# Kernel optimization log

Hardware: AMD Instinct MI355X
Metric: run time of the kernel (lower is better)

## Reference

```python
import jax, jax.numpy as jnp
import numpy as np

N_AGENTS = 16
OBS = 128
STATE = 256
EMBED = 32
NHID = 32
NHEADS = 4
ALPHA = 0.2  # leaky relu slope
NEG = -9.0e15


def gat_layer(h, adj, W, a):
    # h: [B,N,Fin], W: [Fin,Fout], a: [2*Fout,1]  (dropout is identity in eval mode)
    Wh = h @ W                                   # [B,N,Fout]
    f = W.shape[1]
    e = jax.nn.leaky_relu(Wh @ a[:f] + jnp.swapaxes(Wh @ a[f:], 1, 2), ALPHA)  # [B,N,N]
    att = jnp.where(adj > 0, e, NEG)
    att = jax.nn.softmax(att, axis=1)            # faithful to torch dim=1 on [B,N,N]
    return att @ Wh                              # [B,N,Fout]


def gat(x, adj, Wh_heads, a_heads, Wout, aout):
    # Wh_heads: [H,Fin,NHID], a_heads: [H,2*NHID,1]
    heads = jax.vmap(gat_layer, in_axes=(None, None, 0, 0))(x, adj, Wh_heads, a_heads)  # [H,B,N,NHID]
    heads = jax.nn.elu(heads)                    # concat=True layers apply elu
    B, N = x.shape[0], x.shape[1]
    xcat = jnp.transpose(heads, (1, 2, 0, 3)).reshape(B, N, -1)  # [B,N,H*NHID]
    out = gat_layer(xcat, adj, Wout, aout)       # concat=False: no elu inside layer
    out = jax.nn.elu(out)
    return jax.nn.log_softmax(out, axis=1)       # over agent axis, as in torch dim=1


def setup_inputs() -> dict:
    key = jax.random.key(0)
    ks = jax.random.split(key, 20)
    bs, T = 64, 128
    s = 0.05
    inp = {
        "agent_qs": jax.random.normal(ks[0], (bs, T, N_AGENTS), jnp.float32),
        "states": jax.random.normal(ks[1], (bs, T, STATE), jnp.float32),
        "obs_ls": jax.random.normal(ks[2], (bs, T, N_AGENTS, OBS), jnp.float32),
        "adj_ls": jnp.ones((bs, T, N_AGENTS, N_AGENTS), jnp.float32),
        # weight_net: Linear(STATE, N_AGENTS)
        "wn_w": jax.random.normal(ks[3], (N_AGENTS, STATE), jnp.float32) * s,
        "wn_b": jnp.zeros((N_AGENTS,), jnp.float32),
        # hyper_w_1 GAT: 4 heads (OBS->NHID), out (NHID*4 -> N_AGENTS*EMBED)
        "g1_Wh": jax.random.normal(ks[4], (NHEADS, OBS, NHID), jnp.float32) * s,
        "g1_ah": jax.random.normal(ks[5], (NHEADS, 2 * NHID, 1), jnp.float32) * s,
        "g1_Wout": jax.random.normal(ks[6], (NHID * NHEADS, N_AGENTS * EMBED), jnp.float32) * s,
        "g1_aout": jax.random.normal(ks[7], (2 * N_AGENTS * EMBED, 1), jnp.float32) * s,
        # hyper_w_final GAT: 4 heads (OBS->NHID), out (NHID*4 -> EMBED)
        "gf_Wh": jax.random.normal(ks[8], (NHEADS, OBS, NHID), jnp.float32) * s,
        "gf_ah": jax.random.normal(ks[9], (NHEADS, 2 * NHID, 1), jnp.float32) * s,
        "gf_Wout": jax.random.normal(ks[10], (NHID * NHEADS, EMBED), jnp.float32) * s,
        "gf_aout": jax.random.normal(ks[11], (2 * EMBED, 1), jnp.float32) * s,
        # hyper_b_ls: N_AGENTS Linears(STATE -> EMBED), stacked
        "hb_W": jax.random.normal(ks[12], (N_AGENTS, EMBED, STATE), jnp.float32) * s,
        "hb_b": jnp.zeros((N_AGENTS, EMBED), jnp.float32),
        # V: Linear(STATE,EMBED) -> ReLU -> Linear(EMBED,1)
        "v1_w": jax.random.normal(ks[13], (EMBED, STATE), jnp.float32) * s,
        "v1_b": jnp.zeros((EMBED,), jnp.float32),
        "v2_w": jax.random.normal(ks[14], (1, EMBED), jnp.float32) * s,
        "v2_b": jnp.zeros((1,), jnp.float32),
    }
    return inp


def reference(agent_qs, states, obs_ls, adj_ls, wn_w, wn_b,
              g1_Wh, g1_ah, g1_Wout, g1_aout,
              gf_Wh, gf_ah, gf_Wout, gf_aout,
              hb_W, hb_b, v1_w, v1_b, v2_w, v2_b):
    bs = agent_qs.shape[0]
    qs = agent_qs.reshape(-1, N_AGENTS)                 # [B,N]
    st = states.reshape(-1, STATE)                      # [B,S]
    obs = obs_ls.reshape(-1, N_AGENTS, OBS)             # [B,N,OBS]
    adj = adj_ls.reshape(-1, N_AGENTS, N_AGENTS)        # [B,N,N]
    B = qs.shape[0]

    hyper_w1 = jnp.abs(gat(obs, adj, g1_Wh, g1_ah, g1_Wout, g1_aout))   # [B,N,N*E]
    hyper_wf = jnp.abs(gat(obs, adj, gf_Wh, gf_ah, gf_Wout, gf_aout))   # [B,N,E]

    dis = jnp.abs(st @ wn_w.T + wn_b)                   # [B,N]

    w1 = hyper_w1.reshape(B, N_AGENTS, N_AGENTS, EMBED)  # [B,i,n,E]
    b_all = jnp.einsum('bs,nes->bne', st, hb_W) + hb_b   # [B,N,E]
    hidden = jax.nn.elu(jnp.einsum('bn,bine->bie', qs, w1) + b_all)  # [B,N,E]

    v = jax.nn.relu(st @ v1_w.T + v1_b) @ v2_w.T + v2_b  # [B,1]

    y = jnp.einsum('bje,bje->bj', hidden, hyper_wf)       # [B,N]
    q = jnp.einsum('bj,bj->b', y, dis) + v[:, 0]          # [B]
    return q.reshape(bs, -1, 1)
```

## Files before the change

kernel.cpp:

```cpp
#include <hip/hip_runtime.h>
#include <math.h>

#define NAG 16
#define OBSD 128
#define STATED 256
#define ALPHA 0.2f
#define NEGV -9.0e15f
#define BTOT 8192

typedef _Float16 v4h __attribute__((ext_vector_type(4)));
typedef _Float16 v8h __attribute__((ext_vector_type(8)));
typedef float v4f __attribute__((ext_vector_type(4)));

__device__ __forceinline__ float lrelu(float x){ return x > 0.f ? x : ALPHA*x; }
__device__ __forceinline__ float eluf(float x){ return x > 0.f ? x : (__expf(x)-1.f); }

#define MFMA16(A,B,C) __builtin_amdgcn_mfma_f32_16x16x16f16((A),(B),(C),0,0,0)
#define MFMA32(A,B,C) __builtin_amdgcn_mfma_f32_16x16x32_f16((A),(B),(C),0,0,0)

__global__ void prep2_kernel(const float* __restrict__ g1_Wout, const float* __restrict__ g1_aout,
                             const float* __restrict__ gf_Wout, const float* __restrict__ gf_aout,
                             float* __restrict__ wa){
  int k = threadIdx.x;
  float su = 0.f, sv = 0.f;
  for (int c = 0; c < 512; ++c){
    float w = g1_Wout[k*512 + c];
    su += w * g1_aout[c];
    sv += w * g1_aout[512 + c];
  }
  wa[k] = su; wa[128 + k] = sv;
  float fu = 0.f, fv = 0.f;
  for (int c = 0; c < 32; ++c){
    float w = gf_Wout[k*32 + c];
    fu += w * gf_aout[c];
    fv += w * gf_aout[32 + c];
  }
  wa[256 + k] = fu; wa[384 + k] = fv;
}

__global__ void pack_wh_kernel(const float* __restrict__ g1_Wh, const float* __restrict__ gf_Wh,
                               const float* __restrict__ g1_ah, const float* __restrict__ gf_ah,
                               _Float16* __restrict__ dst){
  int idx = blockIdx.x*256 + threadIdx.x;
  if (idx >= 17*2048) return;
  int j = idx & 7, lane = (idx>>3)&63, kk = (idx>>9)&3, nt = idx>>11;
  int k = kk*32 + (lane>>4)*8 + j;
  int li = lane & 15;
  float v;
  if (nt < 16){
    int g = nt>>1, c = (nt&1)*16 + li;
    v = (g<4) ? g1_Wh[(g*OBSD + k)*32 + c] : gf_Wh[((g-4)*OBSD + k)*32 + c];
  } else {
    int g = li>>1, half = li&1;
    const float* W = (g<4)? (g1_Wh + g*OBSD*32) : (gf_Wh + (g-4)*OBSD*32);
    const float* a = ((g<4)? (g1_ah + g*64) : (gf_ah + (g-4)*64)) + half*32;
    float s = 0.f;
    for (int c=0;c<32;++c) s += W[k*32+c]*a[c];
    v = s;
  }
  dst[idx] = (_Float16)v;
}

__global__ void pack_wout_kernel(const float* __restrict__ g1_Wout, const float* __restrict__ gf_Wout,
                                 _Float16* __restrict__ dst1, _Float16* __restrict__ dstf){
  int idx = blockIdx.x*256 + threadIdx.x;
  if (idx < 65536){
    int j = idx&7, lane=(idx>>3)&63, kk=(idx>>9)&3, nt=idx>>11;
    int k = kk*32 + (lane>>4)*8 + j;
    dst1[idx] = (_Float16)g1_Wout[k*512 + nt*16 + (lane&15)];
  } else {
    int i2 = idx - 65536;
    int j=i2&7, lane=(i2>>3)&63, kk=(i2>>9)&3, nt=i2>>11;
    int k = kk*32 + (lane>>4)*8 + j;
    dstf[i2] = (_Float16)gf_Wout[k*32 + nt*16 + (lane&15)];
  }
}

__global__ void pack_wst_kernel(const float* __restrict__ hb_W, const float* __restrict__ wn_w,
                                const float* __restrict__ v1_w, _Float16* __restrict__ dst){
  int idx = blockIdx.x*256 + threadIdx.x;
  if (idx >= 35*4096) return;
  int j = idx&7, lane=(idx>>3)&63, kk=(idx>>9)&7, nt=idx>>12;
  int s = kk*32 + (lane>>4)*8 + j;
  int c = nt*16 + (lane&15);
  float v;
  if (c < 512)      v = hb_W[c*STATED + s];
  else if (c < 528) v = wn_w[(c-512)*STATED + s];
  else              v = v1_w[(c-528)*STATED + s];
  dst[idx] = (_Float16)v;
}

__global__ __launch_bounds__(256) void st_kernel(
    const float* __restrict__ states,
    const _Float16* __restrict__ wstf,
    const float* __restrict__ hb_b, const float* __restrict__ wn_b,
    const float* __restrict__ v1_b, const float* __restrict__ v2_w,
    const float* __restrict__ v2_b,
    float* __restrict__ b_all, float* __restrict__ dis, float* __restrict__ vv){
  __shared__ float vh_s[16*32];
  const int t = threadIdx.x, w = t>>6, lane = t&63, lg = lane>>4, li = lane&15;
  const int b0 = blockIdx.x*16;
  const float* sp = states + (size_t)(b0+li)*STATED + lg*8;
  v8h ast[8];
  #pragma unroll
  for (int kk=0;kk<8;++kk){
    v4f f0 = *reinterpret_cast<const v4f*>(sp + kk*32);
    v4f f1 = *reinterpret_cast<const v4f*>(sp + kk*32 + 4);
    v8h h;
    #pragma unroll
    for (int jj=0;jj<4;++jj){ h[jj]=(_Float16)f0[jj]; h[4+jj]=(_Float16)f1[jj]; }
    ast[kk]=h;
  }
  for (int nt=w; nt<35; nt+=4){
    v4f d = {0.f,0.f,0.f,0.f};
    #pragma unroll
    for (int kk=0;kk<8;++kk){
      v8h bf = *reinterpret_cast<const v8h*>(wstf + (size_t)(((nt*8+kk)<<6)+lane)*8);
      d = MFMA32(ast[kk], bf, d);
    }
    int c = nt*16 + li;
    if (c < 512){
      float bias = hb_b[c];
      #pragma unroll
      for (int r=0;r<4;++r) b_all[(size_t)(b0+lg*4+r)*512 + c] = d[r]+bias;
    } else if (c < 528){
      float bias = wn_b[c-512];
      #pragma unroll
      for (int r=0;r<4;++r) dis[(b0+lg*4+r)*NAG + (c-512)] = fabsf(d[r]+bias);
    } else {
      float bias = v1_b[c-528];
      #pragma unroll
      for (int r=0;r<4;++r) vh_s[(lg*4+r)*32 + (c-528)] = fmaxf(d[r]+bias, 0.f);
    }
  }
  __syncthreads();
  if (t < 16){
    float s = v2_b[0];
    #pragma unroll
    for (int e=0;e<32;++e) s += vh_s[t*32+e]*v2_w[e];
    vv[b0+t] = s;
  }
}

__global__ __launch_bounds__(256,4) void gat_kernel(
    const float* __restrict__ agent_qs,
    const float* __restrict__ obs_ls,
    const float* __restrict__ adj_ls,
    const _Float16* __restrict__ whf,
    const _Float16* __restrict__ wo1f,
    const _Float16* __restrict__ wodf,
    const float* __restrict__ wa_g,
    const float* __restrict__ b_all_ws,
    const float* __restrict__ dis_ws,
    const float* __restrict__ vv_ws,
    float* __restrict__ out){
  __shared__ __align__(16) _Float16 arena_h[16384];
  __shared__ __align__(16) float adj_s[1024];
  __shared__ float qs_s[64];
  __shared__ float y_s[64];

  const int t = threadIdx.x, w = t>>6, lane = t&63, lg = lane>>4, li = lane&15;
  const int bb = blockIdx.x*4;
  const int b = bb + w;
  const v4f ZERO4 = {0.f,0.f,0.f,0.f};

  reinterpret_cast<float4*>(adj_s)[t] =
      reinterpret_cast<const float4*>(adj_ls + (size_t)bb*256)[t];
  if (t < 64) qs_s[t] = agent_qs[bb*NAG + t];

  _Float16* slot   = arena_h + (w<<12);
  _Float16* att_h  = slot;
  float*    uv_f   = reinterpret_cast<float*>(slot + 2176);
  float*    u2v2_f = reinterpret_cast<float*>(slot + 2688);
  float*    att2_f = reinterpret_cast<float*>(slot + 2816);

  const float* ob = obs_ls + (size_t)b*(NAG*OBSD) + li*OBSD + lg*8;
  v8h aob[4];
  #pragma unroll
  for (int kk=0;kk<4;++kk){
    v4f f0 = *reinterpret_cast<const v4f*>(ob + kk*32);
    v4f f1 = *reinterpret_cast<const v4f*>(ob + kk*32 + 4);
    v8h h;
    #pragma unroll
    for (int jj=0;jj<4;++jj){ h[jj]=(_Float16)f0[jj]; h[4+jj]=(_Float16)f1[jj]; }
    aob[kk]=h;
  }
  v4h whB[16];
  #pragma unroll
  for (int nt=0;nt<16;++nt){
    v4f d = ZERO4;
    #pragma unroll
    for (int kk=0;kk<4;++kk){
      v8h bf = *reinterpret_cast<const v8h*>(whf + (size_t)(((nt*4+kk)<<6) + lane)*8);
      d = MFMA32(aob[kk], bf, d);
    }
    v4h hh;
    #pragma unroll
    for (int r=0;r<4;++r) hh[r]=(_Float16)d[r];
    whB[nt]=hh;
  }
  {
    v4f d = ZERO4;
    #pragma unroll
    for (int kk=0;kk<4;++kk){
      v8h bf = *reinterpret_cast<const v8h*>(whf + (size_t)(((64+kk)<<6) + lane)*8);
      d = MFMA32(aob[kk], bf, d);
    }
    #pragma unroll
    for (int r=0;r<4;++r)
      uv_f[(li>>1)*32 + (li&1)*16 + lg*4 + r] = d[r];
  }

  {
    const float* adj_w = adj_s + w*256;
    int cc = lane*2;
    int g = cc>>4, j0 = cc&15;
    float vj0 = uv_f[g*32+16+j0], vj1 = uv_f[g*32+16+j0+1];
    float e0[16], e1[16];
    float m0=-INFINITY, m1=-INFINITY;
    #pragma unroll
    for (int i=0;i<16;++i){
      float u = uv_f[g*32+i];
      float x0 = lrelu(u+vj0), x1 = lrelu(u+vj1);
      x0 = (adj_w[i*16+j0]   > 0.f) ? x0 : NEGV;
      x1 = (adj_w[i*16+j0+1] > 0.f) ? x1 : NEGV;
      e0[i]=x0; e1[i]=x1;
      m0=fmaxf(m0,x0); m1=fmaxf(m1,x1);
    }
    float s0=0.f,s1=0.f;
    #pragma unroll
    for (int i=0;i<16;++i){ e0[i]=__expf(e0[i]-m0); e1[i]=__expf(e1[i]-m1); s0+=e0[i]; s1+=e1[i]; }
    float inv0=1.f/s0, inv1=1.f/s1;
    #pragma unroll
    for (int i=0;i<16;++i){
      union { unsigned u32; _Float16 h[2]; } pk;
      pk.h[0]=(_Float16)(e0[i]*inv0);
      pk.h[1]=(_Float16)(e1[i]*inv1);
      *reinterpret_cast<unsigned*>(&att_h[g*272 + i*16 + j0]) = pk.u32;
    }
  }

  v4h xcB[16];
  float p2[4][4];
  #pragma unroll
  for (int k4=0;k4<4;++k4)
    #pragma unroll
    for (int r=0;r<4;++r) p2[k4][r]=0.f;
  #pragma unroll
  for (int g=0;g<8;++g){
    v4h afr = *reinterpret_cast<const v4h*>(&att_h[g*272 + li*16 + lg*4]);
    int side = g>>2;
    #pragma unroll
    for (int h2=0;h2<2;++h2){
      int nt = g*2+h2;
      v4f d = ZERO4;
      d = MFMA16(afr, whB[nt], d);
      int cl = (nt - side*8)*16 + li;
      float wu = wa_g[side*256 + cl];
      float wv = wa_g[side*256 + 128 + cl];
      v4h hh;
      #pragma unroll
      for (int r=0;r<4;++r){
        float e = eluf(d[r]);
        hh[r]=(_Float16)e;
        p2[side*2][r]   += e*wu;
        p2[side*2+1][r] += e*wv;
      }
      xcB[nt]=hh;
    }
  }
  #pragma unroll
  for (int off=1; off<16; off<<=1)
    #pragma unroll
    for (int k4=0;k4<4;++k4)
      #pragma unroll
      for (int r=0;r<4;++r) p2[k4][r] += __shfl_xor(p2[k4][r], off, 64);
  if (li==0){
    #pragma unroll
    for (int k4=0;k4<4;++k4)
      #pragma unroll
      for (int r=0;r<4;++r) u2v2_f[k4*16 + lg*4 + r] = p2[k4][r];
  }

  if (lane < 32){
    int side = lane>>4, j = lane&15;
    const float* adj_w = adj_s + w*256;
    float vj = u2v2_f[side*32 + 16 + j];
    float ev[16]; float m=-INFINITY;
    #pragma unroll
    for (int i=0;i<16;++i){
      float x = lrelu(u2v2_f[side*32 + i] + vj);
      x = (adj_w[i*16+j] > 0.f) ? x : NEGV;
      ev[i]=x; m=fmaxf(m,x);
    }
    float ss=0.f;
    #pragma unroll
    for (int i=0;i<16;++i){ ev[i]=__expf(ev[i]-m); ss+=ev[i]; }
    float inv=1.f/ss;
    #pragma unroll
    for (int i=0;i<16;++i) att2_f[side*272 + j*17 + i] = ev[i]*inv;
  }

  v4h bat0, bat1;
  #pragma unroll
  for (int jj=0;jj<4;++jj){
    bat0[jj] = (_Float16)att2_f[(lg*4+jj)*17 + li];
    bat1[jj] = (_Float16)att2_f[272 + (lg*4+jj)*17 + li];
  }
  #pragma unroll
  for (int side=0;side<2;++side){
    v4h bat = side ? bat1 : bat0;
    #pragma unroll
    for (int ct=0;ct<8;++ct){
      v4f zD = ZERO4;
      zD = MFMA16(xcB[side*8+ct], bat, zD);
      int kk = ct>>1;
      int lp = li + 16*((ct&1)*2 + (lg>>1));
      _Float16* dst = slot + side*2048 + kk*512 + lp*8 + (lg&1)*4;
      union { unsigned u32; _Float16 h[2]; } q0,q1;
      q0.h[0]=(_Float16)zD[0]; q0.h[1]=(_Float16)zD[1];
      q1.h[0]=(_Float16)zD[2]; q1.h[1]=(_Float16)zD[3];
      *reinterpret_cast<unsigned*>(dst)   = q0.u32;
      *reinterpret_cast<unsigned*>(dst+2) = q1.u32;
    }
  }
  __syncthreads();

  v8h az1[4][4];
  #pragma unroll
  for (int b4=0;b4<4;++b4)
    #pragma unroll
    for (int kk=0;kk<4;++kk)
      az1[b4][kk] = *reinterpret_cast<const v8h*>(arena_h + (b4<<12) + kk*512 + lane*8);
  v8h azf[4];
  #pragma unroll
  for (int kk=0;kk<4;++kk)
    azf[kk] = *reinterpret_cast<const v8h*>(arena_h + (w<<12) + 2048 + kk*512 + lane*8);

  v4f ofD[2];
  #pragma unroll
  for (int nt2=0;nt2<2;++nt2){
    v4f d = ZERO4;
    #pragma unroll
    for (int kk=0;kk<4;++kk){
      v8h bf = *reinterpret_cast<const v8h*>(wodf + (size_t)(((nt2*4+kk)<<6)+lane)*8);
      d = MFMA32(azf[kk], bf, d);
    }
    ofD[nt2]=d;
  }
  __syncthreads();

  float* part = reinterpret_cast<float*>(arena_h);
  float* hyp  = part + 4096;

  #pragma unroll
  for (int nt2=0;nt2<2;++nt2){
    float x[4];
    #pragma unroll
    for (int r=0;r<4;++r) x[r]=eluf(ofD[nt2][r]);
    float m = fmaxf(fmaxf(x[0],x[1]),fmaxf(x[2],x[3]));
    m = fmaxf(m, __shfl_xor(m,16,64));
    m = fmaxf(m, __shfl_xor(m,32,64));
    float s = __expf(x[0]-m)+__expf(x[1]-m)+__expf(x[2]-m)+__expf(x[3]-m);
    s += __shfl_xor(s,16,64);
    s += __shfl_xor(s,32,64);
    float ls = m + __logf(s);
    #pragma unroll
    for (int r=0;r<4;++r)
      hyp[w*512 + (lg*4+r)*32 + nt2*16 + li] = fabsf(x[r]-ls);
  }

  {
    const int base = (w>>1) + ((w&1)<<4);
    float pa[4][4];
    #pragma unroll
    for (int b4=0;b4<4;++b4)
      #pragma unroll
      for (int r=0;r<4;++r) pa[b4][r]=0.f;
    #pragma unroll
    for (int n8=0;n8<8;++n8){
      int nt = base + 2*n8;
      v8h bf[4];
      #pragma unroll
      for (int kk=0;kk<4;++kk)
        bf[kk] = *reinterpret_cast<const v8h*>(wo1f + (size_t)(((nt*4+kk)<<6)+lane)*8);
      #pragma unroll
      for (int b4=0;b4<4;++b4){
        v4f d = ZERO4;
        #pragma unroll
        for (int kk=0;kk<4;++kk) d = MFMA32(az1[b4][kk], bf[kk], d);
        float x[4];
        #pragma unroll
        for (int r=0;r<4;++r) x[r]=eluf(d[r]);
        float m = fmaxf(fmaxf(x[0],x[1]),fmaxf(x[2],x[3]));
        m = fmaxf(m, __shfl_xor(m,16,64));
        m = fmaxf(m, __shfl_xor(m,32,64));
        float s = __expf(x[0]-m)+__expf(x[1]-m)+__expf(x[2]-m)+__expf(x[3]-m);
        s += __shfl_xor(s,16,64);
        s += __shfl_xor(s,32,64);
        float ls = m + __logf(s);
        float q = qs_s[b4*16 + (nt>>1)];
        #pragma unroll
        for (int r=0;r<4;++r) pa[b4][r] += q*fabsf(x[r]-ls);
      }
    }
    #pragma unroll
    for (int b4=0;b4<4;++b4)
      #pragma unroll
      for (int r=0;r<4;++r)
        part[(w*4+b4)*256 + (lg*4+r)*16 + li] = pa[b4][r];
  }
  __syncthreads();

  {
    int b2 = t>>6, i2 = (t>>2)&15, q8 = t&3;
    const float* ba = b_all_ws + (size_t)(bb+b2)*512 + i2*32;
    float ps = 0.f;
    #pragma unroll
    for (int e8=0;e8<8;++e8){
      int e = q8*8 + e8;
      int eh = e>>4;
      float s = ba[e]
              + part[((eh*2  )*4 + b2)*256 + i2*16 + (e&15)]
              + part[((eh*2+1)*4 + b2)*256 + i2*16 + (e&15)];
      ps += eluf(s) * hyp[b2*512 + i2*32 + e];
    }
    ps += __shfl_xor(ps,1,64);
    ps += __shfl_xor(ps,2,64);
    if (q8==0) y_s[b2*16+i2] = ps * dis_ws[(size_t)(bb+b2)*NAG + i2];
  }
  __syncthreads();
  if (t < 4){
    float q = vv_ws[bb+t];
    #pragma unroll
    for (int i=0;i<16;++i) q += y_s[t*16+i];
    out[bb+t] = q;
  }
}

extern "C" void kernel_launch(void* const* d_in, const int* in_sizes, int n_in,
                              void* d_out, int out_size, void* d_ws, size_t ws_size,
                              hipStream_t stream) {
  const float* agent_qs = (const float*)d_in[0];
  const float* states   = (const float*)d_in[1];
  const float* obs_ls   = (const float*)d_in[2];
  const float* adj_ls   = (const float*)d_in[3];
  const float* wn_w     = (const float*)d_in[4];
  const float* wn_b     = (const float*)d_in[5];
  const float* g1_Wh    = (const float*)d_in[6];
  const float* g1_ah    = (const float*)d_in[7];
  const float* g1_Wout  = (const float*)d_in[8];
  const float* g1_aout  = (const float*)d_in[9];
  const float* gf_Wh    = (const float*)d_in[10];
  const float* gf_ah    = (const float*)d_in[11];
  const float* gf_Wout  = (const float*)d_in[12];
  const float* gf_aout  = (const float*)d_in[13];
  const float* hb_W     = (const float*)d_in[14];
  const float* hb_b     = (const float*)d_in[15];
  const float* v1_w     = (const float*)d_in[16];
  const float* v1_b     = (const float*)d_in[17];
  const float* v2_w     = (const float*)d_in[18];
  const float* v2_b     = (const float*)d_in[19];

  float* ws    = (float*)d_ws;
  float* b_all = ws;
  float* dis   = b_all + (size_t)BTOT*512;
  float* vvv   = dis + (size_t)BTOT*NAG;
  float* wa    = vvv + BTOT;
  _Float16* whf  = (_Float16*)(wa + 512);
  _Float16* wo1f = whf + 34816;
  _Float16* wodf = wo1f + 65536;
  _Float16* wstf = wodf + 4096;

  prep2_kernel<<<dim3(1), dim3(128), 0, stream>>>(g1_Wout, g1_aout, gf_Wout, gf_aout, wa);
  pack_wh_kernel<<<dim3(136), dim3(256), 0, stream>>>(g1_Wh, gf_Wh, g1_ah, gf_ah, whf);
  pack_wout_kernel<<<dim3(272), dim3(256), 0, stream>>>(g1_Wout, gf_Wout, wo1f, wodf);
  pack_wst_kernel<<<dim3(560), dim3(256), 0, stream>>>(hb_W, wn_w, v1_w, wstf);
  st_kernel<<<dim3(BTOT/16), dim3(256), 0, stream>>>(states, wstf, hb_b, wn_b, v1_b, v2_w, v2_b,
                                                     b_all, dis, vvv);
  gat_kernel<<<dim3(BTOT/4), dim3(256), 0, stream>>>(agent_qs, obs_ls, adj_ls,
                                                     whf, wo1f, wodf, wa,
                                                     b_all, dis, vvv, (float*)d_out);
}
```

Measured before the change: 134.1 us.

## Shrink LDS footprint and repartition final-layer work to raise occupancy

```diff
diff --git a/kernel.cpp b/kernel.cpp
--- a/kernel.cpp
+++ b/kernel.cpp
@@ -7,6 +7,7 @@
 #define ALPHA 0.2f
 #define NEGV -9.0e15f
 #define BTOT 8192
+#define SLOT_H 3072
 
 typedef _Float16 v4h __attribute__((ext_vector_type(4)));
 typedef _Float16 v8h __attribute__((ext_vector_type(8)));
@@ -142,7 +143,7 @@
   }
 }
 
-__global__ __launch_bounds__(256,4) void gat_kernel(
+__global__ __launch_bounds__(256,6) void gat_kernel(
     const float* __restrict__ agent_qs,
     const float* __restrict__ obs_ls,
     const float* __restrict__ adj_ls,
@@ -154,25 +155,29 @@
     const float* __restrict__ dis_ws,
     const float* __restrict__ vv_ws,
     float* __restrict__ out){
-  __shared__ __align__(16) _Float16 arena_h[16384];
-  __shared__ __align__(16) float adj_s[1024];
+  __shared__ __align__(16) _Float16 arena_h[4*SLOT_H];
+  __shared__ __align__(8)  _Float16 adjh[4*256];
   __shared__ float qs_s[64];
-  __shared__ float y_s[64];
 
   const int t = threadIdx.x, w = t>>6, lane = t&63, lg = lane>>4, li = lane&15;
   const int bb = blockIdx.x*4;
   const int b = bb + w;
+  const int eh = w&1, pb = (w>>1)*2;
   const v4f ZERO4 = {0.f,0.f,0.f,0.f};
 
-  reinterpret_cast<float4*>(adj_s)[t] =
-      reinterpret_cast<const float4*>(adj_ls + (size_t)bb*256)[t];
+  {
+    float4 f = reinterpret_cast<const float4*>(adj_ls + (size_t)bb*256)[t];
+    _Float16* ap = adjh + t*4;
+    ap[0]=(_Float16)f.x; ap[1]=(_Float16)f.y; ap[2]=(_Float16)f.z; ap[3]=(_Float16)f.w;
+  }
   if (t < 64) qs_s[t] = agent_qs[bb*NAG + t];
 
-  _Float16* slot   = arena_h + (w<<12);
+  _Float16* slot   = arena_h + w*SLOT_H;
   _Float16* att_h  = slot;
-  float*    uv_f   = reinterpret_cast<float*>(slot + 2176);
-  float*    u2v2_f = reinterpret_cast<float*>(slot + 2688);
-  float*    att2_f = reinterpret_cast<float*>(slot + 2816);
+  _Float16* uv_h   = slot + 2176;
+  _Float16* u2v2_h = slot + 2432;
+  _Float16* att2_h = slot + 2496;
+  const _Float16* adjw = adjh + w*256;
 
   const float* ob = obs_ls + (size_t)b*(NAG*OBSD) + li*OBSD + lg*8;
   v8h aob[4];
@@ -208,22 +213,23 @@
     }
     #pragma unroll
     for (int r=0;r<4;++r)
-      uv_f[(li>>1)*32 + (li&1)*16 + lg*4 + r] = d[r];
+      uv_h[(li>>1)*32 + (li&1)*16 + lg*4 + r] = (_Float16)d[r];
   }
 
   {
-    const float* adj_w = adj_s + w*256;
     int cc = lane*2;
     int g = cc>>4, j0 = cc&15;
-    float vj0 = uv_f[g*32+16+j0], vj1 = uv_f[g*32+16+j0+1];
+    float vj0 = (float)uv_h[g*32+16+j0], vj1 = (float)uv_h[g*32+16+j0+1];
     float e0[16], e1[16];
     float m0=-INFINITY, m1=-INFINITY;
     #pragma unroll
     for (int i=0;i<16;++i){
-      float u = uv_f[g*32+i];
+      float u = (float)uv_h[g*32+i];
+      union { unsigned u32; _Float16 h[2]; } aa;
+      aa.u32 = *reinterpret_cast<const unsigned*>(adjw + i*16 + j0);
       float x0 = lrelu(u+vj0), x1 = lrelu(u+vj1);
-      x0 = (adj_w[i*16+j0]   > 0.f) ? x0 : NEGV;
-      x1 = (adj_w[i*16+j0+1] > 0.f) ? x1 : NEGV;
+      x0 = ((float)aa.h[0] > 0.f) ? x0 : NEGV;
+      x1 = ((float)aa.h[1] > 0.f) ? x1 : NEGV;
       e0[i]=x0; e1[i]=x1;
       m0=fmaxf(m0,x0); m1=fmaxf(m1,x1);
     }
@@ -236,7 +242,8 @@
       union { unsigned u32; _Float16 h[2]; } pk;
       pk.h[0]=(_Float16)(e0[i]*inv0);
       pk.h[1]=(_Float16)(e1[i]*inv1);
-      *reinterpret_cast<unsigned*>(&att_h[g*272 + i*16 + j0]) = pk.u32;
+      int blk = (j0>>2) ^ ((i>>2)&3);
+      *reinterpret_cast<unsigned*>(&att_h[g*272 + i*16 + (blk<<2) + (j0&3)]) = pk.u32;
     }
   }
 
@@ -246,27 +253,30 @@
   for (int k4=0;k4<4;++k4)
     #pragma unroll
     for (int r=0;r<4;++r) p2[k4][r]=0.f;
-  #pragma unroll
-  for (int g=0;g<8;++g){
-    v4h afr = *reinterpret_cast<const v4h*>(&att_h[g*272 + li*16 + lg*4]);
-    int side = g>>2;
-    #pragma unroll
-    for (int h2=0;h2<2;++h2){
-      int nt = g*2+h2;
-      v4f d = ZERO4;
-      d = MFMA16(afr, whB[nt], d);
-      int cl = (nt - side*8)*16 + li;
-      float wu = wa_g[side*256 + cl];
-      float wv = wa_g[side*256 + 128 + cl];
-      v4h hh;
-      #pragma unroll
-      for (int r=0;r<4;++r){
-        float e = eluf(d[r]);
-        hh[r]=(_Float16)e;
-        p2[side*2][r]   += e*wu;
-        p2[side*2+1][r] += e*wv;
+  {
+    const int ablk = (lg ^ ((li>>2)&3)) << 2;
+    #pragma unroll
+    for (int g=0;g<8;++g){
+      v4h afr = *reinterpret_cast<const v4h*>(&att_h[g*272 + li*16 + ablk]);
+      int side = g>>2;
+      #pragma unroll
+      for (int h2=0;h2<2;++h2){
+        int nt = g*2+h2;
+        v4f d = ZERO4;
+        d = MFMA16(afr, whB[nt], d);
+        int cl = (nt - side*8)*16 + li;
+        float wu = wa_g[side*256 + cl];
+        float wv = wa_g[side*256 + 128 + cl];
+        v4h hh;
+        #pragma unroll
+        for (int r=0;r<4;++r){
+          float e = eluf(d[r]);
+          hh[r]=(_Float16)e;
+          p2[side*2][r]   += e*wu;
+          p2[side*2+1][r] += e*wv;
+        }
+        xcB[nt]=hh;
       }
-      xcB[nt]=hh;
     }
   }
   #pragma unroll
@@ -279,18 +289,17 @@
     #pragma unroll
     for (int k4=0;k4<4;++k4)
       #pragma unroll
-      for (int r=0;r<4;++r) u2v2_f[k4*16 + lg*4 + r] = p2[k4][r];
+      for (int r=0;r<4;++r) u2v2_h[k4*16 + lg*4 + r] = (_Float16)p2[k4][r];
   }
 
   if (lane < 32){
     int side = lane>>4, j = lane&15;
-    const float* adj_w = adj_s + w*256;
-    float vj = u2v2_f[side*32 + 16 + j];
+    float vj = (float)u2v2_h[side*32 + 16 + j];
     float ev[16]; float m=-INFINITY;
     #pragma unroll
     for (int i=0;i<16;++i){
-      float x = lrelu(u2v2_f[side*32 + i] + vj);
-      x = (adj_w[i*16+j] > 0.f) ? x : NEGV;
+      float x = lrelu((float)u2v2_h[side*32 + i] + vj);
+      x = ((float)adjw[i*16+j] > 0.f) ? x : NEGV;
       ev[i]=x; m=fmaxf(m,x);
     }
     float ss=0.f;
@@ -298,46 +307,63 @@
     for (int i=0;i<16;++i){ ev[i]=__expf(ev[i]-m); ss+=ev[i]; }
     float inv=1.f/ss;
     #pragma unroll
-    for (int i=0;i<16;++i) att2_f[side*272 + j*17 + i] = ev[i]*inv;
+    for (int i=0;i<16;++i) att2_h[side*288 + j*18 + i] = (_Float16)(ev[i]*inv);
   }
 
   v4h bat0, bat1;
   #pragma unroll
   for (int jj=0;jj<4;++jj){
-    bat0[jj] = (_Float16)att2_f[(lg*4+jj)*17 + li];
-    bat1[jj] = (_Float16)att2_f[272 + (lg*4+jj)*17 + li];
-  }
-  #pragma unroll
-  for (int side=0;side<2;++side){
-    v4h bat = side ? bat1 : bat0;
-    #pragma unroll
-    for (int ct=0;ct<8;++ct){
-      v4f zD = ZERO4;
-      zD = MFMA16(xcB[side*8+ct], bat, zD);
-      int kk = ct>>1;
-      int lp = li + 16*((ct&1)*2 + (lg>>1));
-      _Float16* dst = slot + side*2048 + kk*512 + lp*8 + (lg&1)*4;
-      union { unsigned u32; _Float16 h[2]; } q0,q1;
-      q0.h[0]=(_Float16)zD[0]; q0.h[1]=(_Float16)zD[1];
-      q1.h[0]=(_Float16)zD[2]; q1.h[1]=(_Float16)zD[3];
-      *reinterpret_cast<unsigned*>(dst)   = q0.u32;
-      *reinterpret_cast<unsigned*>(dst+2) = q1.u32;
-    }
+    bat0[jj] = att2_h[(lg*4+jj)*18 + li];
+    bat1[jj] = att2_h[288 + (lg*4+jj)*18 + li];
+  }
+  #pragma unroll
+  for (int ct=0;ct<8;++ct){
+    v4f zD = ZERO4;
+    zD = MFMA16(xcB[ct], bat0, zD);
+    int kk = ct>>1;
+    int lp = li + 16*((ct&1)*2 + (lg>>1));
+    _Float16* dst = slot + kk*512 + lp*8 + (lg&1)*4;
+    union { unsigned u32; _Float16 h[2]; } q0,q1;
+    q0.h[0]=(_Float16)zD[0]; q0.h[1]=(_Float16)zD[1];
+    q1.h[0]=(_Float16)zD[2]; q1.h[1]=(_Float16)zD[3];
+    *reinterpret_cast<unsigned*>(dst)   = q0.u32;
+    *reinterpret_cast<unsigned*>(dst+2) = q1.u32;
+  }
+  unsigned qg0[8], qg1[8];
+  #pragma unroll
+  for (int ct=0;ct<8;++ct){
+    v4f zD = ZERO4;
+    zD = MFMA16(xcB[8+ct], bat1, zD);
+    union { unsigned u32; _Float16 h[2]; } q0,q1;
+    q0.h[0]=(_Float16)zD[0]; q0.h[1]=(_Float16)zD[1];
+    q1.h[0]=(_Float16)zD[2]; q1.h[1]=(_Float16)zD[3];
+    qg0[ct]=q0.u32; qg1[ct]=q1.u32;
   }
   __syncthreads();
 
-  v8h az1[4][4];
-  #pragma unroll
-  for (int b4=0;b4<4;++b4)
+  v8h az[2][4];
+  #pragma unroll
+  for (int bi=0;bi<2;++bi)
     #pragma unroll
     for (int kk=0;kk<4;++kk)
-      az1[b4][kk] = *reinterpret_cast<const v8h*>(arena_h + (b4<<12) + kk*512 + lane*8);
+      az[bi][kk] = *reinterpret_cast<const v8h*>(arena_h + (pb+bi)*SLOT_H + kk*512 + lane*8);
+  __syncthreads();
+
+  #pragma unroll
+  for (int ct=0;ct<8;++ct){
+    int kk = ct>>1;
+    int lp = li + 16*((ct&1)*2 + (lg>>1));
+    _Float16* dst = slot + kk*512 + lp*8 + (lg&1)*4;
+    *reinterpret_cast<unsigned*>(dst)   = qg0[ct];
+    *reinterpret_cast<unsigned*>(dst+2) = qg1[ct];
+  }
   v8h azf[4];
   #pragma unroll
   for (int kk=0;kk<4;++kk)
-    azf[kk] = *reinterpret_cast<const v8h*>(arena_h + (w<<12) + 2048 + kk*512 + lane*8);
-
-  v4f ofD[2];
+    azf[kk] = *reinterpret_cast<const v8h*>(slot + kk*512 + lane*8);
+  __syncthreads();
+
+  float hyp[2][4];
   #pragma unroll
   for (int nt2=0;nt2<2;++nt2){
     v4f d = ZERO4;
@@ -346,18 +372,9 @@
       v8h bf = *reinterpret_cast<const v8h*>(wodf + (size_t)(((nt2*4+kk)<<6)+lane)*8);
       d = MFMA32(azf[kk], bf, d);
     }
-    ofD[nt2]=d;
-  }
-  __syncthreads();
-
-  float* part = reinterpret_cast<float*>(arena_h);
-  float* hyp  = part + 4096;
-
-  #pragma unroll
-  for (int nt2=0;nt2<2;++nt2){
     float x[4];
     #pragma unroll
-    for (int r=0;r<4;++r) x[r]=eluf(ofD[nt2][r]);
+    for (int r=0;r<4;++r) x[r]=eluf(d[r]);
     float m = fmaxf(fmaxf(x[0],x[1]),fmaxf(x[2],x[3]));
     m = fmaxf(m, __shfl_xor(m,16,64));
     m = fmaxf(m, __shfl_xor(m,32,64));
@@ -366,29 +383,27 @@
     s += __shfl_xor(s,32,64);
     float ls = m + __logf(s);
     #pragma unroll
-    for (int r=0;r<4;++r)
-      hyp[w*512 + (lg*4+r)*32 + nt2*16 + li] = fabsf(x[r]-ls);
+    for (int r=0;r<4;++r) hyp[nt2][r] = fabsf(x[r]-ls);
   }
 
   {
-    const int base = (w>>1) + ((w&1)<<4);
-    float pa[4][4];
-    #pragma unroll
-    for (int b4=0;b4<4;++b4)
-      #pragma unroll
-      for (int r=0;r<4;++r) pa[b4][r]=0.f;
-    #pragma unroll
-    for (int n8=0;n8<8;++n8){
-      int nt = base + 2*n8;
+    float pa[2][4];
+    #pragma unroll
+    for (int bi=0;bi<2;++bi)
+      #pragma unroll
+      for (int r=0;r<4;++r) pa[bi][r]=0.f;
+    #pragma unroll
+    for (int n=0;n<16;++n){
+      int nt = n*2 + eh;
       v8h bf[4];
       #pragma unroll
       for (int kk=0;kk<4;++kk)
         bf[kk] = *reinterpret_cast<const v8h*>(wo1f + (size_t)(((nt*4+kk)<<6)+lane)*8);
       #pragma unroll
-      for (int b4=0;b4<4;++b4){
+      for (int bi=0;bi<2;++bi){
         v4f d = ZERO4;
         #pragma unroll
-        for (int kk=0;kk<4;++kk) d = MFMA32(az1[b4][kk], bf[kk], d);
+        for (int kk=0;kk<4;++kk) d = MFMA32(az[bi][kk], bf[kk], d);
         float x[4];
         #pragma unroll
         for (int r=0;r<4;++r) x[r]=eluf(d[r]);
@@ -399,42 +414,45 @@
         s += __shfl_xor(s,16,64);
         s += __shfl_xor(s,32,64);
         float ls = m + __logf(s);
-        float q = qs_s[b4*16 + (nt>>1)];
+        float q = qs_s[(pb+bi)*16 + n];
         #pragma unroll
-        for (int r=0;r<4;++r) pa[b4][r] += q*fabsf(x[r]-ls);
+        for (int r=0;r<4;++r) pa[bi][r] += q*fabsf(x[r]-ls);
       }
     }
     #pragma unroll
-    for (int b4=0;b4<4;++b4)
-      #pragma unroll
-      for (int r=0;r<4;++r)
-        part[(w*4+b4)*256 + (lg*4+r)*16 + li] = pa[b4][r];
+    for (int bi=0;bi<2;++bi){
+      float* pdst = reinterpret_cast<float*>(arena_h + (pb+bi)*SLOT_H + (eh ? 0 : 2048));
+      #pragma unroll
+      for (int r=0;r<4;++r) pdst[(lg*4+r)*16 + li] = pa[bi][r];
+    }
   }
   __syncthreads();
 
   {
-    int b2 = t>>6, i2 = (t>>2)&15, q8 = t&3;
-    const float* ba = b_all_ws + (size_t)(bb+b2)*512 + i2*32;
-    float ps = 0.f;
-    #pragma unroll
-    for (int e8=0;e8<8;++e8){
-      int e = q8*8 + e8;
-      int eh = e>>4;
-      float s = ba[e]
-              + part[((eh*2  )*4 + b2)*256 + i2*16 + (e&15)]
-              + part[((eh*2+1)*4 + b2)*256 + i2*16 + (e&15)];
-      ps += eluf(s) * hyp[b2*512 + i2*32 + e];
-    }
-    ps += __shfl_xor(ps,1,64);
-    ps += __shfl_xor(ps,2,64);
-    if (q8==0) y_s[b2*16+i2] = ps * dis_ws[(size_t)(bb+b2)*NAG + i2];
-  }
-  __syncthreads();
-  if (t < 4){
-    float q = vv_ws[bb+t];
-    #pragma unroll
-    for (int i=0;i<16;++i) q += y_s[t*16+i];
-    out[bb+t] = q;
+    const float* ph0 = reinterpret_cast<const float*>(slot + 2048);
+    const float* ph1 = reinterpret_cast<const float*>(slot);
+    const float* ba = b_all_ws + (size_t)b*512;
+    float ps[4] = {0.f,0.f,0.f,0.f};
+    #pragma unroll
+    for (int nt2=0;nt2<2;++nt2){
+      const float* ph = nt2 ? ph1 : ph0;
+      #pragma unroll
+      for (int r=0;r<4;++r){
+        int i = lg*4+r;
+        float hv = eluf(ba[i*32 + nt2*16 + li] + ph[i*16 + li]);
+        ps[r] += hv * hyp[nt2][r];
+      }
+    }
+    #pragma unroll
+    for (int off=1; off<16; off<<=1)
+      #pragma unroll
+      for (int r=0;r<4;++r) ps[r] += __shfl_xor(ps[r], off, 64);
+    float qp = 0.f;
+    #pragma unroll
+    for (int r=0;r<4;++r) qp += ps[r] * dis_ws[(size_t)b*NAG + lg*4 + r];
+    qp += __shfl_xor(qp, 16, 64);
+    qp += __shfl_xor(qp, 32, 64);
+    if (lane == 0) out[b] = qp + vv_ws[b];
   }
 }
 
```

After: 363.7 us. +171.3%, slower.
